# Kernel optimization log

Hardware: AMD Instinct MI355X
Metric: run time of the kernel (lower is better)

The kernel has to match this reference:

```python
import jax, jax.numpy as jnp
import numpy as np

N = 100000   # nodes
E = 600000   # edges
F_IN = 128
F_OUT = 128


def setup_inputs() -> dict:
    key = jax.random.key(0)
    k1, k2, k3, k4 = jax.random.split(key, 4)
    x = jax.random.normal(k1, (N, F_IN), dtype=jnp.float32)
    edge_index = jax.random.randint(k2, (2, E), 0, N, dtype=jnp.int32)
    edge_wt = jnp.ones((E,), dtype=jnp.float32)  # learnable param, init ones
    # GCNConv weight (glorot-ish scale) and bias
    weight = jax.random.normal(k3, (F_IN, F_OUT), dtype=jnp.float32) / np.sqrt(F_IN).astype(np.float32)
    bias = jnp.zeros((F_OUT,), dtype=jnp.float32)
    u = jax.random.normal(k4, (F_IN,), dtype=jnp.float32)  # spectral-norm power-iter buffer
    return {"x": x, "edge_index": edge_index, "edge_wt": edge_wt,
            "weight": weight, "bias": bias, "u": u}


def _l2norm(v):
    return v / (jnp.linalg.norm(v) + 1e-12)


def reference(x, edge_index, edge_wt, weight, bias, u):
    # --- spectral norm on GCNConv weight (one power iteration, torch semantics:
    # u, v are stop-gradiented buffers; sigma = u^T W v keeps grad wrt W) ---
    W_sg = jax.lax.stop_gradient(weight)
    v = _l2norm(W_sg.T @ jax.lax.stop_gradient(u))
    u1 = _l2norm(W_sg @ v)
    sigma = u1 @ (weight @ v)
    W_sn = weight / sigma

    # --- per-edge sigmoid-weighted GCNConv with self loops + symmetric norm ---
    w = jax.nn.sigmoid(edge_wt)                      # [E]
    row, col = edge_index[0], edge_index[1]
    loop = jnp.arange(N, dtype=edge_index.dtype)
    row_a = jnp.concatenate([row, loop])             # [E+N]
    col_a = jnp.concatenate([col, loop])
    w_a = jnp.concatenate([w, jnp.ones((N,), w.dtype)])  # self-loop weight 1

    deg = jax.ops.segment_sum(w_a, col_a, num_segments=N)   # [N]
    dinv = jnp.where(deg > 0, deg ** -0.5, 0.0)
    norm = dinv[row_a] * w_a * dinv[col_a]           # [E+N]

    xw = x @ W_sn                                    # [N, F_OUT]
    msgs = norm[:, None] * xw[row_a]                 # [E+N, F_OUT] gather
    out = jax.ops.segment_sum(msgs, col_a, num_segments=N) + bias  # scatter
    return out
```

## Files before the change

### kernel.cpp

```cpp
#include <hip/hip_runtime.h>
#include <math.h>

#define F 128

typedef __bf16 bf16_t;
typedef unsigned long long u64;
typedef __attribute__((ext_vector_type(8))) bf16_t bf16x8;
typedef __attribute__((ext_vector_type(4))) bf16_t bf16x4;
typedef __attribute__((ext_vector_type(4))) float floatx4;

#define DEG_SCALE 8388608.0f
#define DEG_INV   (1.0f / 8388608.0f)

__global__ __launch_bounds__(256) void init_spec_k(const float* __restrict__ W,
                                                   const float* __restrict__ u,
                                                   bf16_t* __restrict__ Wt,
                                                   u64* __restrict__ dc, int n) {
    if (blockIdx.x == 0) {
        __shared__ float sv[F];
        __shared__ float red[F];
        __shared__ float snorm;
        __shared__ float s_is;
        int t = threadIdx.x;
        float s = 0.f;
        if (t < F) {
            for (int i = 0; i < F; ++i) s += W[i * F + t] * u[i];
            red[t] = s * s;
        }
        __syncthreads();
        if (t == 0) {
            float a = 0.f;
            for (int i = 0; i < F; ++i) a += red[i];
            snorm = sqrtf(a);
        }
        __syncthreads();
        if (t < F) sv[t] = s / (snorm + 1e-12f);
        __syncthreads();
        float s2 = 0.f;
        if (t < F) {
            for (int j = 0; j < F; ++j) s2 += W[t * F + j] * sv[j];
            red[t] = s2 * s2;
        }
        __syncthreads();
        if (t == 0) {
            float a = 0.f;
            for (int i = 0; i < F; ++i) a += red[i];
            float nt = sqrtf(a);
            float sigma = a / (nt + 1e-12f);
            s_is = 1.0f / sigma;
        }
        __syncthreads();
        if (t < F) {
            float is = s_is;
            for (int nrow = 0; nrow < F; ++nrow)
                Wt[nrow * F + t] = (bf16_t)(W[t * F + nrow] * is);
        }
    } else {
        int i = (blockIdx.x - 1) * 256 + threadIdx.x;
        if (i < n) dc[i] = 0ULL;
    }
}

#define GBM 64
#define LDK 136
__global__ __launch_bounds__(256) void count_gemm_k(const int* __restrict__ col,
                                                    const float* __restrict__ wt,
                                                    u64* __restrict__ dc, int e_cnt,
                                                    const float* __restrict__ x,
                                                    const bf16_t* __restrict__ Wt,
                                                    bf16_t* __restrict__ xwh, int nrows,
                                                    int gCount) {
    __shared__ bf16_t As[GBM * LDK];
    __shared__ bf16_t Ws[F * LDK];
    int b = blockIdx.x;
    if (b < gCount) {
        int e = b * 256 + threadIdx.x;
        if (e < e_cnt) {
            int c = col[e];
            float w = 1.0f / (1.0f + expf(-wt[e]));
            u64 pkt = (1ULL << 32) | (u64)(unsigned)rintf(w * DEG_SCALE);
            atomicAdd(dc + c, pkt);
        }
        return;
    }
    int tid = threadIdx.x;
    int rowBase = (b - gCount) * GBM;

    for (int i = tid; i < GBM * 32; i += 256) {
        int r = i >> 5, c4 = (i & 31) * 4;
        float4 xv = make_float4(0.f, 0.f, 0.f, 0.f);
        if (rowBase + r < nrows) xv = *(const float4*)(x + (size_t)(rowBase + r) * F + c4);
        bf16x4 v;
        v.x = (bf16_t)xv.x; v.y = (bf16_t)xv.y; v.z = (bf16_t)xv.z; v.w = (bf16_t)xv.w;
        *(bf16x4*)(As + r * LDK + c4) = v;
    }
    for (int i = tid; i < 2048; i += 256) {
        int nrow = i >> 4;
        int c = (i & 15) * 8;
        *(bf16x8*)(Ws + nrow * LDK + c) = *(const bf16x8*)(Wt + nrow * F + c);
    }
    __syncthreads();

    int wave = tid >> 6, lane = tid & 63;
    int l16 = lane & 15, q = lane >> 4;
    int mrow = wave * 16;

    floatx4 acc[8];
#pragma unroll
    for (int nt = 0; nt < 8; ++nt) acc[nt] = (floatx4){0.f, 0.f, 0.f, 0.f};

#pragma unroll
    for (int kt = 0; kt < 4; ++kt) {
        bf16x8 a = *(bf16x8*)(As + (mrow + l16) * LDK + kt * 32 + q * 8);
#pragma unroll
        for (int nt = 0; nt < 8; ++nt) {
            bf16x8 bb = *(bf16x8*)(Ws + (nt * 16 + l16) * LDK + kt * 32 + q * 8);
            acc[nt] = __builtin_amdgcn_mfma_f32_16x16x32_bf16(a, bb, acc[nt], 0, 0, 0);
        }
    }
    __syncthreads();

#pragma unroll
    for (int nt = 0; nt < 8; ++nt) {
#pragma unroll
        for (int r = 0; r < 4; ++r)
            As[(mrow + q * 4 + r) * LDK + nt * 16 + l16] = (bf16_t)acc[nt][r];
    }
    __syncthreads();

    for (int i = tid; i < GBM * 16; i += 256) {
        int r = i >> 4, c = (i & 15) * 8;
        if (rowBase + r < nrows)
            *(bf16x8*)(xwh + (size_t)(rowBase + r) * F + c) = *(bf16x8*)(As + r * LDK + c);
    }
}

#define STILE 1024
__global__ __launch_bounds__(256) void scan1_k(const u64* __restrict__ dc,
                                               int* __restrict__ bsum,
                                               float* __restrict__ dinv, int n) {
    __shared__ int red[256];
    int t = threadIdx.x;
    int base = blockIdx.x * STILE + t * 4;
    int s = 0;
    for (int i = 0; i < 4; ++i) {
        if (base + i < n) {
            u64 v = dc[base + i];
            s += (int)(v >> 32);
            float d = 1.0f + (float)(unsigned)(v & 0xFFFFFFFFULL) * DEG_INV;
            dinv[base + i] = 1.0f / sqrtf(d);
        }
    }
    red[t] = s;
    __syncthreads();
    for (int o = 128; o > 0; o >>= 1) { if (t < o) red[t] += red[t + o]; __syncthreads(); }
    if (t == 0) bsum[blockIdx.x] = red[0];
}

__global__ __launch_bounds__(256) void scan2_k(int* __restrict__ bsum, int g,
                                               int* __restrict__ offsets, int n) {
    int t = threadIdx.x;
    if (g <= 256) {
        __shared__ int s[256];
        int v = (t < g) ? bsum[t] : 0;
        s[t] = v;
        __syncthreads();
        for (int o = 1; o < 256; o <<= 1) {
            int val = s[t];
            int add = (t >= o) ? s[t - o] : 0;
            __syncthreads();
            s[t] = val + add;
            __syncthreads();
        }
        if (t < g) bsum[t] = s[t] - v;
        if (t == g - 1) offsets[n] = s[t];
    } else if (t == 0) {
        int acc = 0;
        for (int i = 0; i < g; ++i) { int v = bsum[i]; bsum[i] = acc; acc += v; }
        offsets[n] = acc;
    }
}

__global__ __launch_bounds__(256) void scan3_k(const u64* __restrict__ dc,
                                               const int* __restrict__ bsum,
                                               int* __restrict__ offsets,
                                               int* __restrict__ cursor, int n) {
    __shared__ int sc[256];
    int t = threadIdx.x;
    int base = blockIdx.x * STILE + t * 4;
    int v[4] = {0, 0, 0, 0};
    for (int i = 0; i < 4; ++i)
        if (base + i < n) v[i] = (int)(dc[base + i] >> 32);
    int ts = v[0] + v[1] + v[2] + v[3];
    sc[t] = ts;
    __syncthreads();
    for (int o = 1; o < 256; o <<= 1) {
        int val = sc[t];
        int add = (t >= o) ? sc[t - o] : 0;
        __syncthreads();
        sc[t] = val + add;
        __syncthreads();
    }
    int run = bsum[blockIdx.x] + sc[t] - ts;
    for (int i = 0; i < 4; ++i) {
        if (base + i < n) { offsets[base + i] = run; cursor[base + i] = run; }
        run += v[i];
    }
}

__global__ __launch_bounds__(256) void fill_k(const int* __restrict__ row,
                                              const int* __restrict__ col,
                                              const float* __restrict__ wt,
                                              const float* __restrict__ dinv,
                                              int* __restrict__ cursor,
                                              int2* __restrict__ edat, int e_cnt) {
    int e = blockIdx.x * 256 + threadIdx.x;
    if (e < e_cnt) {
        int r = row[e], c = col[e];
        float w = 1.0f / (1.0f + expf(-wt[e]));
        float nv = dinv[r] * w * dinv[c];
        int p = atomicAdd(cursor + c, 1);
        edat[p] = make_int2(r, __float_as_int(nv));
    }
}

template <int MODE>
__global__ __launch_bounds__(256) void gather_t(const int* __restrict__ offsets,
                                                const int2* __restrict__ edat,
                                                const float* __restrict__ dinv,
                                                const float* __restrict__ x,
                                                const bf16_t* __restrict__ xh,
                                                const float* __restrict__ bias,
                                                float* __restrict__ out, int n) {
    int node = blockIdx.x * 4 + (threadIdx.x >> 6);
    if (node >= n) return;
    int lane = threadIdx.x & 63;
    const float2* x2 = (const float2*)x;
    float dv = dinv[node];
    float2 acc;
    if (MODE) {
        unsigned vs = ((const unsigned*)(xh + (size_t)node * F))[lane];
        acc.x = dv * dv * __uint_as_float(vs << 16);
        acc.y = dv * dv * __uint_as_float(vs & 0xFFFF0000u);
    } else {
        float2 xv = x2[(size_t)node * 64 + lane];
        acc.x = dv * dv * xv.x;
        acc.y = dv * dv * xv.y;
    }
    int s = offsets[node], e = offsets[node + 1];
    for (int b = s; b < e; b += 64) {
        int cnt = min(64, e - b);
        int2 ed = make_int2(0, 0);
        if (lane < cnt) ed = edat[b + lane];
        int j = 0;
        for (; j + 4 <= cnt; j += 4) {
            int r0 = __shfl(ed.x, j + 0), r1 = __shfl(ed.x, j + 1);
            int r2 = __shfl(ed.x, j + 2), r3 = __shfl(ed.x, j + 3);
            float n0 = __int_as_float(__shfl(ed.y, j + 0));
            float n1 = __int_as_float(__shfl(ed.y, j + 1));
            float n2 = __int_as_float(__shfl(ed.y, j + 2));
            float n3 = __int_as_float(__shfl(ed.y, j + 3));
            if (MODE) {
                unsigned v0 = ((const unsigned*)(xh + (size_t)r0 * F))[lane];
                unsigned v1 = ((const unsigned*)(xh + (size_t)r1 * F))[lane];
                unsigned v2 = ((const unsigned*)(xh + (size_t)r2 * F))[lane];
                unsigned v3 = ((const unsigned*)(xh + (size_t)r3 * F))[lane];
                acc.x = fmaf(n0, __uint_as_float(v0 << 16), acc.x);
                acc.y = fmaf(n0, __uint_as_float(v0 & 0xFFFF0000u), acc.y);
                acc.x = fmaf(n1, __uint_as_float(v1 << 16), acc.x);
                acc.y = fmaf(n1, __uint_as_float(v1 & 0xFFFF0000u), acc.y);
                acc.x = fmaf(n2, __uint_as_float(v2 << 16), acc.x);
                acc.y = fmaf(n2, __uint_as_float(v2 & 0xFFFF0000u), acc.y);
                acc.x = fmaf(n3, __uint_as_float(v3 << 16), acc.x);
                acc.y = fmaf(n3, __uint_as_float(v3 & 0xFFFF0000u), acc.y);
            } else {
                float2 a0 = x2[(size_t)r0 * 64 + lane];
                float2 a1 = x2[(size_t)r1 * 64 + lane];
                float2 a2 = x2[(size_t)r2 * 64 + lane];
                float2 a3 = x2[(size_t)r3 * 64 + lane];
                acc.x = fmaf(n0, a0.x, acc.x); acc.y = fmaf(n0, a0.y, acc.y);
                acc.x = fmaf(n1, a1.x, acc.x); acc.y = fmaf(n1, a1.y, acc.y);
                acc.x = fmaf(n2, a2.x, acc.x); acc.y = fmaf(n2, a2.y, acc.y);
                acc.x = fmaf(n3, a3.x, acc.x); acc.y = fmaf(n3, a3.y, acc.y);
            }
        }
        for (; j < cnt; ++j) {
            int r = __shfl(ed.x, j);
            float nv = __int_as_float(__shfl(ed.y, j));
            if (MODE) {
                unsigned v = ((const unsigned*)(xh + (size_t)r * F))[lane];
                acc.x = fmaf(nv, __uint_as_float(v << 16), acc.x);
                acc.y = fmaf(nv, __uint_as_float(v & 0xFFFF0000u), acc.y);
            } else {
                float2 xr = x2[(size_t)r * 64 + lane];
                acc.x = fmaf(nv, xr.x, acc.x);
                acc.y = fmaf(nv, xr.y, acc.y);
            }
        }
    }
    if (MODE) {
        float2 bv = ((const float2*)bias)[lane];
        acc.x += bv.x;
        acc.y += bv.y;
    }
    ((float2*)out)[(size_t)node * 64 + lane] = acc;
}

__global__ __launch_bounds__(256) void gemm_mfma_k(float* __restrict__ io,
                                                   const bf16_t* __restrict__ Wt,
                                                   const float* __restrict__ bias,
                                                   int nrows) {
    __shared__ bf16_t As[GBM * LDK];
    __shared__ bf16_t Ws[F * LDK];
    int tid = threadIdx.x;
    int rowBase = blockIdx.x * GBM;

    for (int i = tid; i < GBM * 32; i += 256) {
        int r = i >> 5, c4 = (i & 31) * 4;
        float4 xv = make_float4(0.f, 0.f, 0.f, 0.f);
        if (rowBase + r < nrows) xv = *(const float4*)(io + (size_t)(rowBase + r) * F + c4);
        bf16x4 v;
        v.x = (bf16_t)xv.x; v.y = (bf16_t)xv.y; v.z = (bf16_t)xv.z; v.w = (bf16_t)xv.w;
        *(bf16x4*)(As + r * LDK + c4) = v;
    }
    for (int i = tid; i < 2048; i += 256) {
        int nrow = i >> 4;
        int c = (i & 15) * 8;
        *(bf16x8*)(Ws + nrow * LDK + c) = *(const bf16x8*)(Wt + nrow * F + c);
    }
    __syncthreads();

    int wave = tid >> 6, lane = tid & 63;
    int l16 = lane & 15, q = lane >> 4;
    int mrow = wave * 16;

    floatx4 acc[8];
#pragma unroll
    for (int nt = 0; nt < 8; ++nt) acc[nt] = (floatx4){0.f, 0.f, 0.f, 0.f};

#pragma unroll
    for (int kt = 0; kt < 4; ++kt) {
        bf16x8 a = *(bf16x8*)(As + (mrow + l16) * LDK + kt * 32 + q * 8);
#pragma unroll
        for (int nt = 0; nt < 8; ++nt) {
            bf16x8 b = *(bf16x8*)(Ws + (nt * 16 + l16) * LDK + kt * 32 + q * 8);
            acc[nt] = __builtin_amdgcn_mfma_f32_16x16x32_bf16(a, b, acc[nt], 0, 0, 0);
        }
    }

#pragma unroll
    for (int nt = 0; nt < 8; ++nt) {
        int col = nt * 16 + l16;
        float bv = bias[col];
#pragma unroll
        for (int r = 0; r < 4; ++r) {
            int grow = rowBase + mrow + q * 4 + r;
            if (grow < nrows) io[(size_t)grow * F + col] = acc[nt][r] + bv;
        }
    }
}

extern "C" void kernel_launch(void* const* d_in, const int* in_sizes, int n_in,
                              void* d_out, int out_size, void* d_ws, size_t ws_size,
                              hipStream_t stream) {
    const float* x    = (const float*)d_in[0];
    const int*   ei   = (const int*)d_in[1];
    const float* ewt  = (const float*)d_in[2];
    const float* W    = (const float*)d_in[3];
    const float* bias = (const float*)d_in[4];
    const float* u    = (const float*)d_in[5];
    float* out = (float*)d_out;

    int n_nodes = in_sizes[0] / F;
    int e_cnt   = in_sizes[2];
    const int* row = ei;
    const int* col = ei + e_cnt;

    char* wsb = (char*)d_ws;
    float* dinv    = (float*)wsb;
    size_t off = ((size_t)n_nodes * 4 + 15) & ~(size_t)15;
    u64*   dc      = (u64*)(wsb + off);
    off += (size_t)n_nodes * 8;
    int*   offsets = (int*)(wsb + off);
    off += (size_t)(n_nodes + 1) * 4;
    off = (off + 15) & ~(size_t)15;
    int*   cursor  = (int*)(wsb + off);
    off += (size_t)n_nodes * 4;
    int*   bsum    = (int*)(wsb + off);
    off += 512 * 4;
    off = (off + 15) & ~(size_t)15;
    int2*  edat    = (int2*)(wsb + off);
    off += (size_t)e_cnt * 8;
    off = (off + 15) & ~(size_t)15;
    bf16_t* Wt     = (bf16_t*)(wsb + off);
    off += (size_t)F * F * 2;
    bf16_t* xwh    = (bf16_t*)(wsb + off);
    size_t need_bf16 = off + (size_t)n_nodes * F * 2;
    int use_bf16 = (ws_size >= need_bf16);

    int g_scan  = (n_nodes + STILE - 1) / STILE;
    int gCount  = (e_cnt + 255) / 256;
    int gInit   = (n_nodes + 255) / 256;
    int gGemm   = (n_nodes + GBM - 1) / GBM;

    init_spec_k<<<gInit + 1, 256, 0, stream>>>(W, u, Wt, dc, n_nodes);
    if (use_bf16) {
        count_gemm_k<<<gCount + gGemm, 256, 0, stream>>>(col, ewt, dc, e_cnt, x, Wt, xwh,
                                                         n_nodes, gCount);
    } else {
        count_gemm_k<<<gCount, 256, 0, stream>>>(col, ewt, dc, e_cnt, x, Wt, xwh,
                                                 n_nodes, gCount);
    }
    scan1_k<<<g_scan, 256, 0, stream>>>(dc, bsum, dinv, n_nodes);
    scan2_k<<<1, 256, 0, stream>>>(bsum, g_scan, offsets, n_nodes);
    scan3_k<<<g_scan, 256, 0, stream>>>(dc, bsum, offsets, cursor, n_nodes);
    fill_k<<<(e_cnt + 255) / 256, 256, 0, stream>>>(row, col, ewt, dinv, cursor, edat, e_cnt);
    if (use_bf16) {
        gather_t<1><<<(n_nodes + 3) / 4, 256, 0, stream>>>(offsets, edat, dinv, x, xwh, bias,
                                                           out, n_nodes);
    } else {
        gather_t<0><<<(n_nodes + 3) / 4, 256, 0, stream>>>(offsets, edat, dinv, x, xwh, bias,
                                                           out, n_nodes);
        gemm_mfma_k<<<gGemm, 256, 0, stream>>>(out, Wt, bias, n_nodes);
    }
}
```

Measured before the change: 240.7 us.

## Read GEMM weights directly from global memory and schedule GEMM blocks first

The GEMM paths no longer stage the 128x128 bf16 weight tile in LDS. Each MFMA B operand now loads straight from global memory, which should hit in cache because the tile is small. This removes the per-block weight copy and about 34KB of LDS per block, which may allow more blocks per CU. The fused count/GEMM launch is also reordered so GEMM blocks come first and edge-count blocks follow. The trade-off is more global/L2 traffic for the repeated B-fragment loads.

```diff
diff --git a/kernel.cpp b/kernel.cpp
--- a/kernel.cpp
+++ b/kernel.cpp
@@ -69,12 +69,11 @@
                                                     const float* __restrict__ x,
                                                     const bf16_t* __restrict__ Wt,
                                                     bf16_t* __restrict__ xwh, int nrows,
-                                                    int gCount) {
+                                                    int gGemm) {
     __shared__ bf16_t As[GBM * LDK];
-    __shared__ bf16_t Ws[F * LDK];
     int b = blockIdx.x;
-    if (b < gCount) {
-        int e = b * 256 + threadIdx.x;
+    if (b >= gGemm) {
+        int e = (b - gGemm) * 256 + threadIdx.x;
         if (e < e_cnt) {
             int c = col[e];
             float w = 1.0f / (1.0f + expf(-wt[e]));
@@ -84,7 +83,7 @@
         return;
     }
     int tid = threadIdx.x;
-    int rowBase = (b - gCount) * GBM;
+    int rowBase = b * GBM;
 
     for (int i = tid; i < GBM * 32; i += 256) {
         int r = i >> 5, c4 = (i & 31) * 4;
@@ -94,11 +93,6 @@
         v.x = (bf16_t)xv.x; v.y = (bf16_t)xv.y; v.z = (bf16_t)xv.z; v.w = (bf16_t)xv.w;
         *(bf16x4*)(As + r * LDK + c4) = v;
     }
-    for (int i = tid; i < 2048; i += 256) {
-        int nrow = i >> 4;
-        int c = (i & 15) * 8;
-        *(bf16x8*)(Ws + nrow * LDK + c) = *(const bf16x8*)(Wt + nrow * F + c);
-    }
     __syncthreads();
 
     int wave = tid >> 6, lane = tid & 63;
@@ -114,7 +108,7 @@
         bf16x8 a = *(bf16x8*)(As + (mrow + l16) * LDK + kt * 32 + q * 8);
 #pragma unroll
         for (int nt = 0; nt < 8; ++nt) {
-            bf16x8 bb = *(bf16x8*)(Ws + (nt * 16 + l16) * LDK + kt * 32 + q * 8);
+            bf16x8 bb = *(const bf16x8*)(Wt + (size_t)(nt * 16 + l16) * F + kt * 32 + q * 8);
             acc[nt] = __builtin_amdgcn_mfma_f32_16x16x32_bf16(a, bb, acc[nt], 0, 0, 0);
         }
     }
@@ -311,7 +305,6 @@
                                                    const float* __restrict__ bias,
                                                    int nrows) {
     __shared__ bf16_t As[GBM * LDK];
-    __shared__ bf16_t Ws[F * LDK];
     int tid = threadIdx.x;
     int rowBase = blockIdx.x * GBM;
 
@@ -323,11 +316,6 @@
         v.x = (bf16_t)xv.x; v.y = (bf16_t)xv.y; v.z = (bf16_t)xv.z; v.w = (bf16_t)xv.w;
         *(bf16x4*)(As + r * LDK + c4) = v;
     }
-    for (int i = tid; i < 2048; i += 256) {
-        int nrow = i >> 4;
-        int c = (i & 15) * 8;
-        *(bf16x8*)(Ws + nrow * LDK + c) = *(const bf16x8*)(Wt + nrow * F + c);
-    }
     __syncthreads();
 
     int wave = tid >> 6, lane = tid & 63;
@@ -343,7 +331,7 @@
         bf16x8 a = *(bf16x8*)(As + (mrow + l16) * LDK + kt * 32 + q * 8);
 #pragma unroll
         for (int nt = 0; nt < 8; ++nt) {
-            bf16x8 b = *(bf16x8*)(Ws + (nt * 16 + l16) * LDK + kt * 32 + q * 8);
+            bf16x8 b = *(const bf16x8*)(Wt + (size_t)(nt * 16 + l16) * F + kt * 32 + q * 8);
             acc[nt] = __builtin_amdgcn_mfma_f32_16x16x32_bf16(a, b, acc[nt], 0, 0, 0);
         }
     }
@@ -405,11 +393,11 @@
 
     init_spec_k<<<gInit + 1, 256, 0, stream>>>(W, u, Wt, dc, n_nodes);
     if (use_bf16) {
-        count_gemm_k<<<gCount + gGemm, 256, 0, stream>>>(col, ewt, dc, e_cnt, x, Wt, xwh,
-                                                         n_nodes, gCount);
+        count_gemm_k<<<gGemm + gCount, 256, 0, stream>>>(col, ewt, dc, e_cnt, x, Wt, xwh,
+                                                         n_nodes, gGemm);
     } else {
         count_gemm_k<<<gCount, 256, 0, stream>>>(col, ewt, dc, e_cnt, x, Wt, xwh,
-                                                 n_nodes, gCount);
+                                                 n_nodes, 0);
     }
     scan1_k<<<g_scan, 256, 0, stream>>>(dc, bsum, dinv, n_nodes);
     scan2_k<<<1, 256, 0, stream>>>(bsum, g_scan, offsets, n_nodes);
```

New measurement: 239.8 us. No clear change (-0.3%).
